# Kernel optimization log

Hardware: AMD Instinct MI355X
Metric: run time of the kernel (lower is better)

Reference implementation:

```python
import jax, jax.numpy as jnp
import numpy as np

HIDDEN = 512


def setup_inputs() -> dict:
    key = jax.random.key(0)
    k1, k2, k3, k4, k5 = jax.random.split(key, 5)
    scale = 1.0 / np.sqrt(HIDDEN)
    return {
        "decoder_hidden": jax.random.normal(k1, (64, HIDDEN), dtype=jnp.float32),
        "encoder_outputs": jax.random.normal(k2, (4096, 64, HIDDEN), dtype=jnp.float32),
        "W1": jax.random.uniform(k3, (HIDDEN, HIDDEN), jnp.float32, -scale, scale),
        "W2": jax.random.uniform(k4, (HIDDEN, HIDDEN), jnp.float32, -scale, scale),
        "v": jax.random.uniform(k5, (HIDDEN,), jnp.float32, -scale, scale),
    }


def reference(decoder_hidden, encoder_outputs, W1, W2, v):
    # decoder_hidden: (B, H); encoder_outputs: (S, B, H)
    enc = jnp.transpose(encoder_outputs, (1, 0, 2))          # (B, S, H)
    dec_proj = decoder_hidden @ W1.T                          # (B, H) — no need to repeat over S
    enc_proj = jnp.einsum('bsh,gh->bsg', enc, W2)             # (B, S, H)
    energy = jnp.tanh(dec_proj[:, None, :] + enc_proj) @ v    # (B, S)
    attn_weights = jax.nn.softmax(energy, axis=1)             # (B, S)
    context = jnp.einsum('bs,bsh->bh', attn_weights, enc)     # (B, H)
    return (context, attn_weights)
```

## Files before the change

kernel.cpp:

```cpp
#include <hip/hip_runtime.h>
#include <math.h>


#define BATCH 64
#define SEQ   4096
#define HID   512

typedef __attribute__((ext_vector_type(8))) short bf16x8;
typedef __attribute__((ext_vector_type(4))) float f32x4;

__device__ __forceinline__ float fast_tanh(float x) {
    return 1.0f - 2.0f / (__expf(2.0f * x) + 1.0f);
}

__device__ __forceinline__ unsigned cvt2(float lo, float hi) {
    unsigned r;
    asm("v_cvt_pk_bf16_f32 %0, %1, %2" : "=v"(r) : "v"(lo), "v"(hi));
    return r;
}

__global__ void k_cvtW2(const float* __restrict__ W2, ushort* __restrict__ W2t)
{
    const int n  = blockIdx.x * 256 + threadIdx.x;
    const int g  = n >> 6, kc = n & 63;
    const int kb = kc >> 2, rgl = kc & 3;
    const int wn = g >> 6, fn = (g >> 4) & 3, gl = g & 15;

    const float* src = W2 + (size_t)g * HID + kc * 8;
    const float4 x = *reinterpret_cast<const float4*>(src);
    const float4 y = *reinterpret_cast<const float4*>(src + 4);
    uint4 u;
    u.x = cvt2(x.x, x.y);  u.y = cvt2(x.z, x.w);
    u.z = cvt2(y.x, y.y);  u.w = cvt2(y.z, y.w);

    const size_t dst = (size_t)kb * 16384 + wn * 2048 + fn * 512
                     + (rgl * 16 + gl) * 8;
    *reinterpret_cast<uint4*>(W2t + dst) = u;
}

__global__ void k_decproj(const float* __restrict__ dh,
                          const float* __restrict__ W1,
                          float* __restrict__ dp)
{
    __shared__ float wrow[HID];
    const int g = blockIdx.x;
    const int t = threadIdx.x;
    for (int i = t; i < HID; i += 256) wrow[i] = W1[g * HID + i];
    __syncthreads();

    const int b = t >> 2, q = t & 3;
    const float* dhb = dh + b * HID + q * 128;
    const float* wr  = wrow + q * 128;
    float acc = 0.f;
    #pragma unroll 8
    for (int i = 0; i < 128; i += 4) {
        const float4 d4 = *reinterpret_cast<const float4*>(dhb + i);
        acc = fmaf(d4.x, wr[i + 0], acc);
        acc = fmaf(d4.y, wr[i + 1], acc);
        acc = fmaf(d4.z, wr[i + 2], acc);
        acc = fmaf(d4.w, wr[i + 3], acc);
    }
    acc += __shfl_xor(acc, 1);
    acc += __shfl_xor(acc, 2);
    if (q == 0) dp[b * HID + g] = acc;
}

__global__ __launch_bounds__(512, 2)
void k_energy(const float* __restrict__ enc, const ushort* __restrict__ W2t,
              const float* __restrict__ dp,  const float* __restrict__ v,
              float* __restrict__ energy)
{
    __shared__ __align__(16) ushort As[64 * 512];
    __shared__ float part[8][64];

    const int idx    = blockIdx.x;
    const int schunk = idx & 63;
    const int b      = idx >> 6;
    const int s0     = schunk * 64;

    const int t    = threadIdx.x;
    const int lane = t & 63;
    const int w    = t >> 6;
    const int gl   = lane & 15, rg = lane >> 4;

    #pragma unroll
    for (int r = 0; r < 8; ++r) {
        const int row = r * 8 + w;
        const float* rp = enc + ((size_t)(s0 + row) * BATCH + b) * HID + lane * 8;
        const float4 x = *reinterpret_cast<const float4*>(rp);
        const float4 y = *reinterpret_cast<const float4*>(rp + 4);
        uint4 u;
        u.x = cvt2(x.x, x.y);  u.y = cvt2(x.z, x.w);
        u.z = cvt2(y.x, y.y);  u.w = cvt2(y.z, y.w);
        const int slot = lane ^ (row & 7);
        *reinterpret_cast<uint4*>(
            reinterpret_cast<char*>(As) + row * 1024 + slot * 16) = u;
    }
    __syncthreads();

    f32x4 acc[4][4];
    const f32x4 z = {0.f, 0.f, 0.f, 0.f};
    #pragma unroll
    for (int m = 0; m < 4; ++m)
        #pragma unroll
        for (int n = 0; n < 4; ++n) acc[m][n] = z;

    const char* asbase = reinterpret_cast<const char*>(As) + gl * 1024;
    const char* bbase  = reinterpret_cast<const char*>(W2t)
                       + w * 4096 + lane * 16;
    const int   gmask  = gl & 7;

    bf16x8 af[2][4], bfr[2][4];

    {
        #pragma unroll
        for (int n = 0; n < 4; ++n)
            bfr[0][n] = *reinterpret_cast<const bf16x8*>(bbase + n * 1024);
        const char* arow = asbase + ((rg) ^ gmask) * 16;
        #pragma unroll
        for (int m = 0; m < 4; ++m)
            af[0][m] = *reinterpret_cast<const bf16x8*>(arow + m * 16384);
    }

    #pragma unroll
    for (int kb = 0; kb < 16; ++kb) {
        const int cur = kb & 1, nxt = cur ^ 1;

        if (kb < 15) {
            const char* bstep = bbase + (kb + 1) * 32768;
            #pragma unroll
            for (int n = 0; n < 4; ++n)
                bfr[nxt][n] = *reinterpret_cast<const bf16x8*>(bstep + n * 1024);
            const char* arow = asbase + ((4 * (kb + 1) + rg) ^ gmask) * 16;
            #pragma unroll
            for (int m = 0; m < 4; ++m)
                af[nxt][m] = *reinterpret_cast<const bf16x8*>(arow + m * 16384);
        }

        __builtin_amdgcn_sched_barrier(0);

        #pragma unroll
        for (int m = 0; m < 4; ++m)
            #pragma unroll
            for (int n = 0; n < 4; ++n)
                acc[m][n] = __builtin_amdgcn_mfma_f32_16x16x32_bf16(
                    af[cur][m], bfr[cur][n], acc[m][n], 0, 0, 0);

        __builtin_amdgcn_sched_barrier(0);
    }

    float dpv[4], vv[4];
    #pragma unroll
    for (int n = 0; n < 4; ++n) {
        const int g = w * 64 + n * 16 + gl;
        dpv[n] = dp[b * HID + g];
        vv[n]  = v[g];
    }
    float p[4][4];
    #pragma unroll
    for (int m = 0; m < 4; ++m)
        #pragma unroll
        for (int r = 0; r < 4; ++r) p[m][r] = 0.f;
    #pragma unroll
    for (int n = 0; n < 4; ++n)
        #pragma unroll
        for (int m = 0; m < 4; ++m)
            #pragma unroll
            for (int r = 0; r < 4; ++r)
                p[m][r] += fast_tanh(dpv[n] + acc[m][n][r]) * vv[n];

    #pragma unroll
    for (int m = 0; m < 4; ++m)
        #pragma unroll
        for (int r = 0; r < 4; ++r) {
            float x = p[m][r];
            x += __shfl_xor(x, 1);
            x += __shfl_xor(x, 2);
            x += __shfl_xor(x, 4);
            x += __shfl_xor(x, 8);
            p[m][r] = x;
        }
    if (gl == 0) {
        #pragma unroll
        for (int m = 0; m < 4; ++m)
            #pragma unroll
            for (int r = 0; r < 4; ++r)
                part[w][m * 16 + rg * 4 + r] = p[m][r];
    }
    __syncthreads();

    if (t < 64) {
        float e = 0.f;
        #pragma unroll
        for (int q = 0; q < 8; ++q) e += part[q][t];
        energy[(size_t)b * SEQ + s0 + t] = e;
    }
}

__global__ void k_softmax(float* __restrict__ attn)
{
    __shared__ float redm[4], reds[4];
    const int b = blockIdx.x, t = threadIdx.x;
    float* e = attn + (size_t)b * SEQ;

    float4 ev[4];
    float m = -3.4e38f;
    #pragma unroll
    for (int i = 0; i < 4; ++i) {
        ev[i] = *reinterpret_cast<const float4*>(e + i * 1024 + t * 4);
        m = fmaxf(m, fmaxf(fmaxf(ev[i].x, ev[i].y), fmaxf(ev[i].z, ev[i].w)));
    }
    #pragma unroll
    for (int off = 1; off < 64; off <<= 1) m = fmaxf(m, __shfl_xor(m, off));
    if ((t & 63) == 0) redm[t >> 6] = m;
    __syncthreads();
    m = fmaxf(fmaxf(redm[0], redm[1]), fmaxf(redm[2], redm[3]));

    float s = 0.f;
    #pragma unroll
    for (int i = 0; i < 4; ++i) {
        ev[i].x = __expf(ev[i].x - m);  ev[i].y = __expf(ev[i].y - m);
        ev[i].z = __expf(ev[i].z - m);  ev[i].w = __expf(ev[i].w - m);
        s += (ev[i].x + ev[i].y) + (ev[i].z + ev[i].w);
    }
    #pragma unroll
    for (int off = 1; off < 64; off <<= 1) s += __shfl_xor(s, off);
    if ((t & 63) == 0) reds[t >> 6] = s;
    __syncthreads();
    s = (reds[0] + reds[1]) + (reds[2] + reds[3]);
    const float inv = 1.0f / s;

    #pragma unroll
    for (int i = 0; i < 4; ++i) {
        const float4 w4 = make_float4(ev[i].x * inv, ev[i].y * inv,
                                      ev[i].z * inv, ev[i].w * inv);
        *reinterpret_cast<float4*>(e + i * 1024 + t * 4) = w4;
    }
}

__global__ void k_ctxpart(const float* __restrict__ enc,
                          const float* __restrict__ attn,
                          float* __restrict__ pctx)
{
    __shared__ float w[256];
    const int b  = blockIdx.x;
    const int sp = blockIdx.y;
    const int t  = threadIdx.x;

    w[t] = attn[(size_t)b * SEQ + sp * 256 + t];
    __syncthreads();

    const float2* e2 = reinterpret_cast<const float2*>(enc);
    size_t idx = ((size_t)sp * 256 * BATCH + b) * (HID / 2) + t;
    const size_t stride = (size_t)BATCH * (HID / 2);

    float ax = 0.f, ay = 0.f;
    #pragma unroll 4
    for (int s = 0; s < 256; ++s) {
        const float2 ev = e2[idx];
        const float ws = w[s];
        ax = fmaf(ws, ev.x, ax);
        ay = fmaf(ws, ev.y, ay);
        idx += stride;
    }
    float2* p2 = reinterpret_cast<float2*>(pctx);
    p2[((size_t)sp * BATCH + b) * (HID / 2) + t] = make_float2(ax, ay);
}

__global__ void k_ctxsum(const float* __restrict__ pctx,
                         float* __restrict__ ctx)
{
    const int i = blockIdx.x * 256 + threadIdx.x;
    float s = 0.f;
    #pragma unroll
    for (int sp = 0; sp < 16; ++sp) s += pctx[(size_t)sp * BATCH * HID + i];
    ctx[i] = s;
}

extern "C" void kernel_launch(void* const* d_in, const int* in_sizes, int n_in,
                              void* d_out, int out_size, void* d_ws, size_t ws_size,
                              hipStream_t stream)
{
    const float* dh  = (const float*)d_in[0];
    const float* enc = (const float*)d_in[1];
    const float* W1  = (const float*)d_in[2];
    const float* W2  = (const float*)d_in[3];
    const float* v   = (const float*)d_in[4];

    float* out  = (float*)d_out;
    float* ctx  = out;
    float* attn = out + BATCH * HID;

    float*  dp   = (float*)d_ws;
    ushort* W2t  = (ushort*)(dp + BATCH * HID);
    float*  pctx = (float*)(W2t + HID * HID);

    k_cvtW2  <<<128, 256, 0, stream>>>(W2, W2t);
    k_decproj<<<HID, 256, 0, stream>>>(dh, W1, dp);
    k_energy <<<4096, 512, 0, stream>>>(enc, W2t, dp, v, attn);
    k_softmax<<<BATCH, 256, 0, stream>>>(attn);
    k_ctxpart<<<dim3(BATCH, 16), 256, 0, stream>>>(enc, attn, pctx);
    k_ctxsum <<<BATCH * HID / 256, 256, 0, stream>>>(pctx, ctx);
}
```

Before: 362.3 us.

## Stream encoder tile into LDS per k-block overlapping MFMA compute

Instead of loading and converting the whole 64x512 encoder tile into shared memory before the MFMA loop, each thread now prefetches fp32 chunks two k-blocks ahead and writes converted bf16 slices into LDS inside the main loop. The goal is to hide global load latency behind the matrix-multiply work rather than stalling on a full upfront load. This adds a workgroup barrier and LDS wait every k-iteration, and removes the sched_barrier hints, which may cost synchronization overhead.

Result: slower. 421.3 us (+16.3%).

```diff
diff --git a/kernel.cpp b/kernel.cpp
--- a/kernel.cpp
+++ b/kernel.cpp
@@ -83,20 +83,13 @@
     const int w    = t >> 6;
     const int gl   = lane & 15, rg = lane >> 4;
 
-    #pragma unroll
-    for (int r = 0; r < 8; ++r) {
-        const int row = r * 8 + w;
-        const float* rp = enc + ((size_t)(s0 + row) * BATCH + b) * HID + lane * 8;
-        const float4 x = *reinterpret_cast<const float4*>(rp);
-        const float4 y = *reinterpret_cast<const float4*>(rp + 4);
-        uint4 u;
-        u.x = cvt2(x.x, x.y);  u.y = cvt2(x.z, x.w);
-        u.z = cvt2(y.x, y.y);  u.w = cvt2(y.z, y.w);
-        const int slot = lane ^ (row & 7);
-        *reinterpret_cast<uint4*>(
-            reinterpret_cast<char*>(As) + row * 1024 + slot * 16) = u;
-    }
-    __syncthreads();
+    const int srow = t >> 3;
+    const int qh   = (t & 7) >> 1;
+    const int half = t & 1;
+    const float* aptr = enc + ((size_t)(s0 + srow) * BATCH + b) * HID
+                      + qh * 8 + half * 4;
+    char* awbase = reinterpret_cast<char*>(As) + srow * 1024 + half * 8;
+    const int rmask = srow & 7;
 
     f32x4 acc[4][4];
     const f32x4 z = {0.f, 0.f, 0.f, 0.f};
@@ -111,33 +104,56 @@
     const int   gmask  = gl & 7;
 
     bf16x8 af[2][4], bfr[2][4];
+    float4 ar0, ar1;
 
     {
-        #pragma unroll
-        for (int n = 0; n < 4; ++n)
-            bfr[0][n] = *reinterpret_cast<const bf16x8*>(bbase + n * 1024);
-        const char* arow = asbase + ((rg) ^ gmask) * 16;
-        #pragma unroll
-        for (int m = 0; m < 4; ++m)
-            af[0][m] = *reinterpret_cast<const bf16x8*>(arow + m * 16384);
-    }
+        const float4 p0 = *reinterpret_cast<const float4*>(aptr);
+        const float4 p1 = *reinterpret_cast<const float4*>(aptr + 32);
+        uint2 u0, u1;
+        u0.x = cvt2(p0.x, p0.y);  u0.y = cvt2(p0.z, p0.w);
+        u1.x = cvt2(p1.x, p1.y);  u1.y = cvt2(p1.z, p1.w);
+        *reinterpret_cast<uint2*>(awbase + ((qh)     ^ rmask) * 16) = u0;
+        *reinterpret_cast<uint2*>(awbase + ((4 + qh) ^ rmask) * 16) = u1;
+    }
+    ar0 = *reinterpret_cast<const float4*>(aptr + 2 * 32);
+    ar1 = *reinterpret_cast<const float4*>(aptr + 3 * 32);
+    #pragma unroll
+    for (int n = 0; n < 4; ++n)
+        bfr[0][n] = *reinterpret_cast<const bf16x8*>(bbase + n * 1024);
+    asm volatile("s_waitcnt lgkmcnt(0)" ::: "memory");
+    __builtin_amdgcn_s_barrier();
+    #pragma unroll
+    for (int m = 0; m < 4; ++m)
+        af[0][m] = *reinterpret_cast<const bf16x8*>(
+            asbase + ((rg) ^ gmask) * 16 + m * 16384);
 
     #pragma unroll
     for (int kb = 0; kb < 16; ++kb) {
         const int cur = kb & 1, nxt = cur ^ 1;
 
-        if (kb < 15) {
+        if (kb <= 13) {
+            const float4 p = cur ? ar1 : ar0;
+            uint2 u;
+            u.x = cvt2(p.x, p.y);  u.y = cvt2(p.z, p.w);
+            *reinterpret_cast<uint2*>(
+                awbase + (((kb + 2) * 4 + qh) ^ rmask) * 16) = u;
+        }
+        if (kb <= 11) {
+            if (cur) ar1 = *reinterpret_cast<const float4*>(aptr + (kb + 4) * 32);
+            else     ar0 = *reinterpret_cast<const float4*>(aptr + (kb + 4) * 32);
+        }
+        if (kb <= 14) {
             const char* bstep = bbase + (kb + 1) * 32768;
             #pragma unroll
             for (int n = 0; n < 4; ++n)
                 bfr[nxt][n] = *reinterpret_cast<const bf16x8*>(bstep + n * 1024);
+        }
+        if (kb <= 14) {
             const char* arow = asbase + ((4 * (kb + 1) + rg) ^ gmask) * 16;
             #pragma unroll
             for (int m = 0; m < 4; ++m)
                 af[nxt][m] = *reinterpret_cast<const bf16x8*>(arow + m * 16384);
         }
-
-        __builtin_amdgcn_sched_barrier(0);
 
         #pragma unroll
         for (int m = 0; m < 4; ++m)
@@ -146,7 +162,8 @@
                 acc[m][n] = __builtin_amdgcn_mfma_f32_16x16x32_bf16(
                     af[cur][m], bfr[cur][n], acc[m][n], 0, 0, 0);
 
-        __builtin_amdgcn_sched_barrier(0);
+        asm volatile("s_waitcnt lgkmcnt(0)" ::: "memory");
+        __builtin_amdgcn_s_barrier();
     }
 
     float dpv[4], vv[4];
@@ -192,7 +209,7 @@
     if (t < 64) {
         float e = 0.f;
         #pragma unroll
-        for (int q = 0; q < 8; ++q) e += part[q][t];
+        for (int q2 = 0; q2 < 8; ++q2) e += part[q2][t];
         energy[(size_t)b * SEQ + s0 + t] = e;
     }
 }
```
